# Performance work log

Hardware: AMD Instinct MI355X
Metric: run time of the kernel (lower is better)

## Reference

```python
import jax, jax.numpy as jnp
import numpy as np

B, T, D, H, L = 256, 128, 512, 512, 3  # batch, T, input_size, hidden_size, lstm layers (D == H so W_ih stacks)


def setup_inputs() -> dict:
    key = jax.random.key(0)
    ks = jax.random.split(key, 7)
    s = 0.05
    return {
        "input_data": jax.random.normal(ks[0], (B, T - 1, D), jnp.float32),
        "W_ih": jax.random.normal(ks[1], (L, 4 * H, D), jnp.float32) * s,
        "W_hh": jax.random.normal(ks[2], (L, 4 * H, H), jnp.float32) * s,
        "b_ih": jax.random.normal(ks[3], (L, 4 * H), jnp.float32) * s,
        "b_hh": jax.random.normal(ks[4], (L, 4 * H), jnp.float32) * s,
        "attn_w": jax.random.normal(ks[5], (2 * H + T - 1, 1), jnp.float32) * s,
        "attn_b": jax.random.normal(ks[6], (1,), jnp.float32) * s,
    }


def _lstm_step(x, h, c, W_ih, W_hh, b_ih, b_hh):
    # single time step of a 3-layer LSTM, PyTorch gate order (i, f, g, o)
    hs, cs = [], []
    inp = x
    for l in range(L):
        gates = inp @ W_ih[l].T + b_ih[l] + h[l] @ W_hh[l].T + b_hh[l]  # [B, 4H]
        i, f, g, o = jnp.split(gates, 4, axis=-1)
        i = jax.nn.sigmoid(i)
        f = jax.nn.sigmoid(f)
        o = jax.nn.sigmoid(o)
        g = jnp.tanh(g)
        c_new = f * c[l] + i * g
        h_new = o * jnp.tanh(c_new)
        hs.append(h_new)
        cs.append(c_new)
        inp = h_new
    return jnp.stack(hs), jnp.stack(cs)


def reference(input_data, W_ih, W_hh, b_ih, b_hh, attn_w, attn_b):
    x_perm = input_data.transpose(0, 2, 1)  # [B, D, T-1], constant across steps
    h0 = jnp.zeros((L, B, H), input_data.dtype)
    c0 = jnp.zeros_like(h0)
    xs = input_data.transpose(1, 0, 2)  # [T-1, B, D]

    def step(carry, x_t):
        h, c = carry
        # input attention uses layer-0 hidden/cell states, as in the original
        hb = jnp.broadcast_to(h[0][:, None, :], (B, D, H))
        cb = jnp.broadcast_to(c[0][:, None, :], (B, D, H))
        feat = jnp.concatenate([hb, cb, x_perm], axis=2)  # [B, D, 2H+T-1]
        logits = (feat @ attn_w)[..., 0] + attn_b[0]      # [B, D]
        attn = jax.nn.softmax(logits, axis=1)
        weighted = attn * x_t                              # [B, D]
        h, c = _lstm_step(weighted, h, c, W_ih, W_hh, b_ih, b_hh)
        return (h, c), (weighted, h[-1])

    _, (input_weighted, input_encoded) = jax.lax.scan(step, (h0, c0), xs)
    # [T-1, B, .] -> [B, T-1, .]
    return input_weighted.transpose(1, 0, 2), input_encoded.transpose(1, 0, 2)
```

## Files before the change

### kernel.cpp

```cpp
#include <hip/hip_runtime.h>
#include <math.h>

#define BATCH 256
#define TT    127
#define DD    512
#define HH    512
#define GG    2048
#define NWG   256
#define NTHR  256
#define OUT0_ELEMS ((size_t)BATCH * TT * DD)

typedef __attribute__((ext_vector_type(8))) short  short8;
typedef __attribute__((ext_vector_type(4))) float  floatx4;
typedef __attribute__((ext_vector_type(4))) unsigned int uintx4;

__device__ __forceinline__ float bf2f(unsigned short u) {
    unsigned int x = ((unsigned int)u) << 16;
    return __builtin_bit_cast(float, x);
}
__device__ __forceinline__ unsigned short f2bf(float f) {
    unsigned int x = __builtin_bit_cast(unsigned int, f);
    unsigned int lsb = (x >> 16) & 1u;
    x += 0x7fffu + lsb;
    return (unsigned short)(x >> 16);
}

__device__ __forceinline__ int detect_is_f32(const unsigned short* p) {
    int cnt = 0;
    for (int i = 0; i < 64; ++i) {
        int e = (p[2 * i] >> 7) & 0xFF;
        cnt += (e >= 112 && e <= 133) ? 1 : 0;
    }
    return cnt < 32;
}

__device__ __forceinline__ short8 load_a8(const void* base, size_t off, int f32m) {
    if (!f32m) return *(const short8*)((const unsigned short*)base + off);
    const float* fp = (const float*)base + off;
    short8 r;
#pragma unroll
    for (int j = 0; j < 8; ++j) r[j] = (short)f2bf(fp[j]);
    return r;
}

__device__ __forceinline__ short8 load_h16(const unsigned short* p) {
    uintx4 r;
    asm volatile("global_load_dwordx4 %0, %1, off sc0 sc1"
                 : "=v"(r) : "v"(p));
    return __builtin_bit_cast(short8, r);
}

__global__ __launch_bounds__(256) void prep_kernel(
    const void* __restrict__ W_ih, const void* __restrict__ W_hh,
    const void* __restrict__ b_ih, const void* __restrict__ b_hh,
    const unsigned short* __restrict__ x_u,
    unsigned short* __restrict__ wih_bf, unsigned short* __restrict__ whh_bf,
    float* __restrict__ bsum, int* __restrict__ flag_ws)
{
    __shared__ int sflag;
    if (threadIdx.x == 0) sflag = detect_is_f32(x_u);
    __syncthreads();
    const int f32m = sflag;
    const int gid = blockIdx.x * 256 + threadIdx.x;
    const int gsz = gridDim.x * 256;
    if (gid == 0) *flag_ws = f32m;

    for (int i = gid; i < 3 * GG; i += gsz) {
        float bi = f32m ? ((const float*)b_ih)[i] : bf2f(((const unsigned short*)b_ih)[i]);
        float bh = f32m ? ((const float*)b_hh)[i] : bf2f(((const unsigned short*)b_hh)[i]);
        bsum[i] = bi + bh;
    }
    if (f32m) {
        const float* wi = (const float*)W_ih;
        const float* wh = (const float*)W_hh;
        const int n = 3 * GG * DD;
        for (int i = gid; i < n; i += gsz) {
            wih_bf[i] = f2bf(wi[i]);
            whh_bf[i] = f2bf(wh[i]);
        }
    }
}

__global__ __launch_bounds__(512) void attn_kernel(
    const void* __restrict__ xv,
    const void* __restrict__ attn_wv,
    void* __restrict__ outv,
    const int* __restrict__ flag_ws)
{
    __shared__ float red[512];
    __shared__ float wx[TT];
    __shared__ int sflag;
    const int b = blockIdx.x;
    const int d = threadIdx.x;
    if (d == 0) sflag = *flag_ws;
    __syncthreads();
    const int f32m = sflag;

    if (d < TT)
        wx[d] = f32m ? ((const float*)attn_wv)[2 * HH + d]
                     : bf2f(((const unsigned short*)attn_wv)[2 * HH + d]);
    __syncthreads();

    const size_t xb = (size_t)b * TT * DD;
    float s = 0.f;
    for (int t = 0; t < TT; ++t) {
        size_t ix = xb + (size_t)t * DD + d;
        float xval = f32m ? ((const float*)xv)[ix] : bf2f(((const unsigned short*)xv)[ix]);
        s += xval * wx[t];
    }

    red[d] = s; __syncthreads();
    for (int off = 256; off > 0; off >>= 1) {
        if (d < off) red[d] = fmaxf(red[d], red[d + off]);
        __syncthreads();
    }
    const float m = red[0]; __syncthreads();
    const float e = expf(s - m);
    red[d] = e; __syncthreads();
    for (int off = 256; off > 0; off >>= 1) {
        if (d < off) red[d] += red[d + off];
        __syncthreads();
    }
    const float a = e / red[0];

    for (int t = 0; t < TT; ++t) {
        size_t ix = xb + (size_t)t * DD + d;
        float xval = f32m ? ((const float*)xv)[ix] : bf2f(((const unsigned short*)xv)[ix]);
        float v = a * xval;
        if (f32m) ((float*)outv)[ix] = v;
        else      ((unsigned short*)outv)[ix] = f2bf(v);
    }
}

__global__ __launch_bounds__(256, 1) void lstm_kernel(
    void* __restrict__ outv,
    const unsigned short* __restrict__ W_ih_o,
    const unsigned short* __restrict__ W_hh_o,
    const unsigned short* __restrict__ wih_bf,
    const unsigned short* __restrict__ whh_bf,
    const float* __restrict__ bsum,
    unsigned short* __restrict__ h_ws,
    unsigned* __restrict__ bar,
    const int* __restrict__ flag_ws)
{
    __shared__ float g_lds[16 * 16 * 33];
    __shared__ int sflag;
    __shared__ int s_dead;

    const int tid = threadIdx.x;
    if (tid == 0) { sflag = *flag_ws; s_dead = 0; }
    __syncthreads();
    const int f32m = sflag;

    const unsigned short* WiB = f32m ? wih_bf : W_ih_o;
    const unsigned short* WhB = f32m ? whh_bf : W_hh_o;

    const int lane   = tid & 63;
    const int wv     = tid >> 6;
    const int m_lane = lane & 15;
    const int kq     = lane >> 4;

    const int blk = blockIdx.x;
    const int xcd = blk & 7;
    const int loc = blk >> 3;
    const int hi  = xcd * 4 + (loc & 3);
    const int bi  = loc >> 2;
    const int hid0 = hi * 16;
    const int b0   = bi * 32;

    const int ep_bl = tid >> 3;
    const int ep_hp = tid & 7;

    float c_reg[3][2];
#pragma unroll
    for (int l = 0; l < 3; ++l) { c_reg[l][0] = 0.f; c_reg[l][1] = 0.f; }

    unsigned* arrv = bar + (size_t)bi * 128;
    unsigned* gen  = bar + (size_t)bi * 128 + 64;

    for (int k = 0; k < TT + 2; ++k) {
        short8 pfb[3][4][2];
#pragma unroll
        for (int j = 0; j < 3; ++j) {
            const int kj = k - j;
            if (kj < 0 || kj > TT) continue;
            const unsigned short* hb =
                h_ws + ((size_t)j * 2 + ((kj - 1) & 1)) * BATCH * HH;
#pragma unroll
            for (int kk = 0; kk < 4; ++kk) {
                const int k0 = (wv * 4 + kk) * 32 + kq * 8;
                pfb[j][kk][0] = load_h16(hb + (size_t)(b0 + m_lane) * HH + k0);
                pfb[j][kk][1] = load_h16(hb + (size_t)(b0 + 16 + m_lane) * HH + k0);
            }
        }
        asm volatile("s_waitcnt vmcnt(0)" ::: "memory");
        __builtin_amdgcn_sched_barrier(0);

#pragma unroll
        for (int l = 0; l < 3; ++l) {
            const int t = k - l;
            if (t < 0 || t >= TT) continue;

            const unsigned short* Wi = WiB + (size_t)l * GG * DD;
            const unsigned short* Wh = WhB + (size_t)l * GG * DD;

            floatx4 acc[2][4];
#pragma unroll
            for (int mt = 0; mt < 2; ++mt)
#pragma unroll
                for (int g = 0; g < 4; ++g) {
                    floatx4 z = {0.f, 0.f, 0.f, 0.f};
                    acc[mt][g] = z;
                }

#pragma unroll
            for (int kk = 0; kk < 4; ++kk) {
                const int k0 = (wv * 4 + kk) * 32 + kq * 8;
                short8 a0, a1;
                if (l == 0) {
                    a0 = load_a8(outv, ((size_t)(b0 + m_lane) * TT + t) * DD + k0, f32m);
                    a1 = load_a8(outv, ((size_t)(b0 + 16 + m_lane) * TT + t) * DD + k0, f32m);
                } else {
                    a0 = pfb[l - 1][kk][0];
                    a1 = pfb[l - 1][kk][1];
                }
#pragma unroll
                for (int g = 0; g < 4; ++g) {
                    short8 bfr = *(const short8*)(Wi + (size_t)(g * HH + hid0 + m_lane) * DD + k0);
                    acc[0][g] = __builtin_amdgcn_mfma_f32_16x16x32_bf16(a0, bfr, acc[0][g], 0, 0, 0);
                    acc[1][g] = __builtin_amdgcn_mfma_f32_16x16x32_bf16(a1, bfr, acc[1][g], 0, 0, 0);
                }
                short8 h0f = pfb[l][kk][0];
                short8 h1f = pfb[l][kk][1];
#pragma unroll
                for (int g = 0; g < 4; ++g) {
                    short8 bfr = *(const short8*)(Wh + (size_t)(g * HH + hid0 + m_lane) * DD + k0);
                    acc[0][g] = __builtin_amdgcn_mfma_f32_16x16x32_bf16(h0f, bfr, acc[0][g], 0, 0, 0);
                    acc[1][g] = __builtin_amdgcn_mfma_f32_16x16x32_bf16(h1f, bfr, acc[1][g], 0, 0, 0);
                }
            }

            __syncthreads();
#pragma unroll
            for (int mt = 0; mt < 2; ++mt)
#pragma unroll
                for (int g = 0; g < 4; ++g)
#pragma unroll
                    for (int r = 0; r < 4; ++r)
                        g_lds[((wv * 4 + g) * 16 + m_lane) * 33 + mt * 16 + kq * 4 + r]
                            = acc[mt][g][r];
            __syncthreads();

            {
                float hout[2];
#pragma unroll
                for (int dlt = 0; dlt < 2; ++dlt) {
                    const int hid = 2 * ep_hp + dlt;
                    float gv[4];
#pragma unroll
                    for (int g = 0; g < 4; ++g) {
                        float sum = 0.f;
#pragma unroll
                        for (int q = 0; q < 4; ++q)
                            sum += g_lds[((q * 4 + g) * 16 + hid) * 33 + ep_bl];
                        sum += bsum[l * GG + g * HH + hid0 + hid];
                        gv[g] = sum;
                    }
                    const float ig = 1.f / (1.f + expf(-gv[0]));
                    const float fg = 1.f / (1.f + expf(-gv[1]));
                    const float gg = tanhf(gv[2]);
                    const float og = 1.f / (1.f + expf(-gv[3]));
                    const float cnew = fg * c_reg[l][dlt] + ig * gg;
                    c_reg[l][dlt] = cnew;
                    hout[dlt] = og * tanhf(cnew);
                }
                const int bgl  = b0 + ep_bl;
                const int hidg = hid0 + 2 * ep_hp;
                const unsigned hpk = (unsigned)f2bf(hout[0])
                                   | ((unsigned)f2bf(hout[1]) << 16);
                __hip_atomic_store(
                    (unsigned*)(h_ws + (((size_t)l * 2 + (t & 1)) * BATCH + bgl) * HH + hidg),
                    hpk, __ATOMIC_RELAXED, __HIP_MEMORY_SCOPE_AGENT);
                if (l == 2) {
                    const size_t ox = OUT0_ELEMS + ((size_t)bgl * TT + t) * HH + hidg;
                    if (f32m) {
                        ((float*)outv)[ox]     = hout[0];
                        ((float*)outv)[ox + 1] = hout[1];
                    } else {
                        *(unsigned*)((unsigned short*)outv + ox) = hpk;
                    }
                }
            }
        }

        if (k < TT + 1) {
            __syncthreads();
            if (tid == 0) {
                if (!s_dead) {
                    asm volatile("s_waitcnt vmcnt(0)" ::: "memory");
                    unsigned arrived = __hip_atomic_fetch_add(arrv, 1u,
                                            __ATOMIC_RELAXED, __HIP_MEMORY_SCOPE_AGENT);
                    if (arrived == (unsigned)(k * 32 + 31)) {
                        __hip_atomic_fetch_add(gen, 1u,
                                           __ATOMIC_RELAXED, __HIP_MEMORY_SCOPE_AGENT);
                    } else {
                        int spins = 0;
                        while (__hip_atomic_load(gen, __ATOMIC_RELAXED,
                                                 __HIP_MEMORY_SCOPE_AGENT)
                               <= (unsigned)k) {
                            __builtin_amdgcn_s_sleep(2);
                            if (++spins > 8000000) { s_dead = 1; break; }
                        }
                    }
                }
            }
            __syncthreads();
        }
    }
}

#define WIH_OFF  ((size_t)0)
#define WIH_SZ   ((size_t)3 * GG * DD * 2)
#define WHH_OFF  (WIH_OFF + WIH_SZ)
#define WHH_SZ   WIH_SZ
#define BSUM_OFF (WHH_OFF + WHH_SZ)
#define BSUM_SZ  ((size_t)3 * GG * 4)
#define H_OFF    (BSUM_OFF + BSUM_SZ)
#define H_SZ     ((size_t)3 * 2 * BATCH * HH * 2)
#define BAR_OFF  (H_OFF + H_SZ)
#define BAR_SZ   ((size_t)4096)
#define FLAG_OFF (BAR_OFF + BAR_SZ)
#define WS_NEED  (FLAG_OFF + 256)

extern "C" void kernel_launch(void* const* d_in, const int* in_sizes, int n_in,
                              void* d_out, int out_size, void* d_ws, size_t ws_size,
                              hipStream_t stream) {
    (void)in_sizes; (void)n_in; (void)out_size;

    const void* x      = d_in[0];
    const void* W_ih   = d_in[1];
    const void* W_hh   = d_in[2];
    const void* b_ih   = d_in[3];
    const void* b_hh   = d_in[4];
    const void* attn_w = d_in[5];

    char* ws = (char*)d_ws;
    unsigned short* wih_bf = (unsigned short*)(ws + WIH_OFF);
    unsigned short* whh_bf = (unsigned short*)(ws + WHH_OFF);
    float*          bsum   = (float*)(ws + BSUM_OFF);
    unsigned short* h_ws   = (unsigned short*)(ws + H_OFF);
    unsigned*       bar    = (unsigned*)(ws + BAR_OFF);
    int*            flagp  = (int*)(ws + FLAG_OFF);

    if (ws_size < WS_NEED) return;

    hipMemsetAsync(ws + H_OFF, 0, H_SZ + BAR_SZ + 256, stream);

    prep_kernel<<<dim3(1024), dim3(256), 0, stream>>>(
        W_ih, W_hh, b_ih, b_hh, (const unsigned short*)x,
        wih_bf, whh_bf, bsum, flagp);

    attn_kernel<<<dim3(BATCH), dim3(512), 0, stream>>>(x, attn_w, d_out, flagp);

    lstm_kernel<<<dim3(NWG), dim3(NTHR), 0, stream>>>(
        d_out, (const unsigned short*)W_ih, (const unsigned short*)W_hh,
        wih_bf, whh_bf, bsum, h_ws, bar, flagp);
}
```

Baseline: 4.271 ms.

## Replace atomic-counter grid barrier with per-block flag slots and leader fan-out

Replaces the per-batch-group barrier, which used a shared atomic fetch-add counter plus a generation word, with per-workgroup arrival flags in separate 2KB slots. A leader workgroup (hi==0) polls all 32 arrival slots in parallel with one wavefront and then writes 32 wake flags. The aim is to remove contended atomic RMWs on one cache line, at the cost of an extra hop through the leader and a larger barrier workspace. The spin-timeout limits and sleep interval also change.

```diff
diff --git a/kernel.cpp b/kernel.cpp
--- a/kernel.cpp
+++ b/kernel.cpp
@@ -9,6 +9,7 @@
 #define NWG   256
 #define NTHR  256
 #define OUT0_ELEMS ((size_t)BATCH * TT * DD)
+#define BARSLOT   2048
 
 typedef __attribute__((ext_vector_type(8))) short  short8;
 typedef __attribute__((ext_vector_type(4))) float  floatx4;
@@ -167,6 +168,15 @@
     const int bi  = loc >> 2;
     const int hid0 = hi * 16;
     const int b0   = bi * 32;
+    const int leader = (hi == 0);
+
+    char* barc = (char*)bar;
+    unsigned* arr_my  = (unsigned*)(barc + (size_t)(bi * 32 + hi) * BARSLOT);
+    unsigned* wake_my = (unsigned*)(barc + (size_t)(256 + bi * 32 + hi) * BARSLOT);
+    unsigned* poll_slot = (unsigned*)(barc +
+        (size_t)(bi * 32 + (tid < 32 ? tid : 31)) * BARSLOT);
+    unsigned* wake_slot = (unsigned*)(barc +
+        (size_t)(256 + bi * 32 + (tid < 32 ? tid : 31)) * BARSLOT);
 
     const int ep_bl = tid >> 3;
     const int ep_hp = tid & 7;
@@ -174,9 +184,6 @@
     float c_reg[3][2];
 #pragma unroll
     for (int l = 0; l < 3; ++l) { c_reg[l][0] = 0.f; c_reg[l][1] = 0.f; }
-
-    unsigned* arrv = bar + (size_t)bi * 128;
-    unsigned* gen  = bar + (size_t)bi * 128 + 64;
 
     for (int k = 0; k < TT + 2; ++k) {
         short8 pfb[3][4][2];
@@ -295,22 +302,36 @@
 
         if (k < TT + 1) {
             __syncthreads();
-            if (tid == 0) {
-                if (!s_dead) {
+            if (!s_dead) {
+                if (tid == 0) {
                     asm volatile("s_waitcnt vmcnt(0)" ::: "memory");
-                    unsigned arrived = __hip_atomic_fetch_add(arrv, 1u,
-                                            __ATOMIC_RELAXED, __HIP_MEMORY_SCOPE_AGENT);
-                    if (arrived == (unsigned)(k * 32 + 31)) {
-                        __hip_atomic_fetch_add(gen, 1u,
-                                           __ATOMIC_RELAXED, __HIP_MEMORY_SCOPE_AGENT);
-                    } else {
+                    __hip_atomic_store(arr_my, (unsigned)(k + 1),
+                                       __ATOMIC_RELAXED, __HIP_MEMORY_SCOPE_AGENT);
+                }
+                if (leader) {
+                    if (tid < 64) {
                         int spins = 0;
-                        while (__hip_atomic_load(gen, __ATOMIC_RELAXED,
-                                                 __HIP_MEMORY_SCOPE_AGENT)
-                               <= (unsigned)k) {
-                            __builtin_amdgcn_s_sleep(2);
-                            if (++spins > 8000000) { s_dead = 1; break; }
+                        for (;;) {
+                            unsigned v = __hip_atomic_load(poll_slot,
+                                __ATOMIC_RELAXED, __HIP_MEMORY_SCOPE_AGENT);
+                            if (__all(v > (unsigned)k)) break;
+                            __builtin_amdgcn_s_sleep(4);
+                            if (++spins > 2000000) {
+                                if (tid == 0) s_dead = 1;
+                                break;
+                            }
                         }
+                        if (tid < 32)
+                            __hip_atomic_store(wake_slot, (unsigned)(k + 1),
+                                __ATOMIC_RELAXED, __HIP_MEMORY_SCOPE_AGENT);
+                    }
+                } else if (tid == 0) {
+                    int spins = 0;
+                    while (__hip_atomic_load(wake_my, __ATOMIC_RELAXED,
+                                             __HIP_MEMORY_SCOPE_AGENT)
+                           <= (unsigned)k) {
+                        __builtin_amdgcn_s_sleep(4);
+                        if (++spins > 2000000) { s_dead = 1; break; }
                     }
                 }
             }
@@ -328,7 +349,7 @@
 #define H_OFF    (BSUM_OFF + BSUM_SZ)
 #define H_SZ     ((size_t)3 * 2 * BATCH * HH * 2)
 #define BAR_OFF  (H_OFF + H_SZ)
-#define BAR_SZ   ((size_t)4096)
+#define BAR_SZ   ((size_t)512 * BARSLOT)
 #define FLAG_OFF (BAR_OFF + BAR_SZ)
 #define WS_NEED  (FLAG_OFF + 256)
 
```

After: 4.252 ms. Within noise of the previous version (-0.4%).
